# Kernel tuning notes

Hardware: AMD Instinct MI355X
Metric: run time of the kernel (lower is better)

Reference implementation:

```python
import jax, jax.numpy as jnp
import numpy as np

N_NODES = 50000
N_EDGES = 800000
D_IN = 64
D_OUT = 64


def setup_inputs() -> dict:
    key = jax.random.key(0)
    k1, k2, k3, k4, k5 = jax.random.split(key, 5)
    x = jax.random.normal(k1, (N_NODES, D_IN), dtype=jnp.float32)
    senders = jax.random.randint(k2, (N_EDGES,), 0, N_NODES, dtype=jnp.int32)
    receivers = jax.random.randint(k3, (N_EDGES,), 0, N_NODES, dtype=jnp.int32)
    # eqx.nn.Linear params: weight [out, in], bias [out]
    weight = jax.random.normal(k4, (D_OUT, D_IN), dtype=jnp.float32) / np.sqrt(D_IN)
    bias = jax.random.normal(k5, (D_OUT,), dtype=jnp.float32) * 0.01
    return {"x": x, "senders": senders, "receivers": receivers, "weight": weight, "bias": bias}


def reference(x, senders, receivers, weight, bias):
    n = x.shape[0]
    # jraph.GraphConvolution applies update_node_fn (the Linear) FIRST
    h = x @ weight.T + bias  # [N, D_OUT]
    # add self edges
    self_idx = jnp.arange(n, dtype=senders.dtype)
    cs = jnp.concatenate([senders, self_idx])
    cr = jnp.concatenate([receivers, self_idx])
    ones = jnp.ones(cs.shape, dtype=h.dtype)
    sender_deg = jax.ops.segment_sum(ones, cs, num_segments=n)
    receiver_deg = jax.ops.segment_sum(ones, cr, num_segments=n)
    # symmetric normalization: D^{-1/2} A D^{-1/2}
    h = h * jax.lax.rsqrt(jnp.maximum(sender_deg, 1.0))[:, None]
    h = jax.ops.segment_sum(h[cs], cr, num_segments=n)  # gather -> scatter-add
    h = h * jax.lax.rsqrt(jnp.maximum(receiver_deg, 1.0))[:, None]
    return jax.nn.leaky_relu(h)  # default negative_slope=0.01
```

## Files before the change

### kernel.cpp

```cpp
#include <hip/hip_runtime.h>

#define N_NODES 50000
#define N_EDGES 800000
#define D 64
#define NB 196
#define BSZ 256
#define NSLICE 256
#define SLICE_I4 784
#define E4 (N_EDGES / 4)
#define CAP 52

__device__ __forceinline__ ushort f2bf(float f) {
    unsigned u = __float_as_uint(f);
    unsigned r = u + 0x7fffu + ((u >> 16) & 1u);
    return (ushort)(r >> 16);
}
__device__ __forceinline__ void acc8(const uint4 a, float* acc) {
    acc[0] += __uint_as_float(a.x << 16);
    acc[1] += __uint_as_float(a.x & 0xffff0000u);
    acc[2] += __uint_as_float(a.y << 16);
    acc[3] += __uint_as_float(a.y & 0xffff0000u);
    acc[4] += __uint_as_float(a.z << 16);
    acc[5] += __uint_as_float(a.z & 0xffff0000u);
    acc[6] += __uint_as_float(a.w << 16);
    acc[7] += __uint_as_float(a.w & 0xffff0000u);
}

__global__ __launch_bounds__(1024) void part1_kernel(
        const int* __restrict__ s, const int* __restrict__ r,
        unsigned* __restrict__ prc, unsigned char* __restrict__ psc,
        int* __restrict__ rcnt, int* __restrict__ scnt) {
    __shared__ int rcur[NB], scur[NB];
    const int tid = threadIdx.x, sl = blockIdx.x;
    for (int i = tid; i < NB; i += 1024) { rcur[i] = 0; scur[i] = 0; }
    __syncthreads();

    const size_t cellbase = (size_t)sl * NB * CAP;
    int e4 = sl * SLICE_I4 + tid;
    if (tid < SLICE_I4 && e4 < E4) {
        int4 rv = ((const int4*)r)[e4];
        int4 sv = ((const int4*)s)[e4];
        int ri[4] = {rv.x, rv.y, rv.z, rv.w};
        int si[4] = {sv.x, sv.y, sv.z, sv.w};
        #pragma unroll
        for (int k = 0; k < 4; ++k) {
            int b = ri[k] >> 8;
            int pos = atomicAdd(&rcur[b], 1);
            if (pos < CAP)
                prc[cellbase + (size_t)b * CAP + pos] =
                    ((unsigned)(ri[k] & 255) << 16) | (unsigned)si[k];
            int bs = si[k] >> 8;
            int pos2 = atomicAdd(&scur[bs], 1);
            if (pos2 < CAP)
                psc[cellbase + (size_t)bs * CAP + pos2] = (unsigned char)(si[k] & 255);
        }
    }
    __syncthreads();
    for (int i = tid; i < NB; i += 1024) {
        rcnt[sl * NB + i] = rcur[i];
        scnt[sl * NB + i] = scur[i];
    }
}

__global__ __launch_bounds__(256, 4) void post_kernel(
        const unsigned* __restrict__ prc, const unsigned char* __restrict__ psc,
        const int* __restrict__ rcnt, const int* __restrict__ scnt,
        int* __restrict__ rowoff, ushort* __restrict__ csr16,
        const float* __restrict__ x, const float* __restrict__ w,
        const float* __restrict__ bias, ushort* __restrict__ h16) {
    __shared__ int sc[256];
    __shared__ int h4[BSZ];
    __shared__ float wlds[64 * 68];
    __shared__ float xlds[64 * 68];
    __shared__ float slds[BSZ];
    __shared__ float blds[64];
    const int tid = threadIdx.x;

    if (blockIdx.x >= NB) {
        const int b = blockIdx.x - NB;
        h4[tid] = 0;
        if (tid < 64) blds[tid] = bias[tid];
        __syncthreads();
        {
            int sl = tid;
            int c = scnt[sl * NB + b];
            const unsigned char* cell = psc + (size_t)sl * NB * CAP + (size_t)b * CAP;
            for (int i = 0; i < c; ++i) atomicAdd(&h4[cell[i]], 1);
        }
        __syncthreads();
        slds[tid] = rsqrtf((float)(h4[tid] + 1));
        #pragma unroll
        for (int q = 0; q < 4; ++q) {
            int idx = q * 256 + tid;
            int o = idx >> 4, k4 = idx & 15;
            float4 wv = ((const float4*)w)[idx];
            *(float4*)&wlds[o * 68 + k4 * 4] = wv;
        }
        __syncthreads();

        const int t15 = tid & 15;
        const int g = tid >> 4;
        for (int tile = 0; tile < 4; ++tile) {
            const int nb = b * BSZ + tile * 64;
            #pragma unroll
            for (int q = 0; q < 4; ++q) {
                int idx = q * 256 + tid;
                int nl = idx >> 4, k4 = idx & 15;
                int n = nb + nl;
                float4 xv = (n < N_NODES) ? ((const float4*)x)[n * 16 + k4]
                                          : make_float4(0.f, 0.f, 0.f, 0.f);
                *(float4*)&xlds[nl * 68 + k4 * 4] = xv;
            }
            __syncthreads();

            float acc[4][4];
            #pragma unroll
            for (int i = 0; i < 4; ++i)
                #pragma unroll
                for (int j = 0; j < 4; ++j) acc[i][j] = 0.f;

            #pragma unroll 2
            for (int k4 = 0; k4 < 16; ++k4) {
                float4 wv0 = *(const float4*)&wlds[(t15     ) * 68 + k4 * 4];
                float4 wv1 = *(const float4*)&wlds[(t15 + 16) * 68 + k4 * 4];
                float4 wv2 = *(const float4*)&wlds[(t15 + 32) * 68 + k4 * 4];
                float4 wv3 = *(const float4*)&wlds[(t15 + 48) * 68 + k4 * 4];
                #pragma unroll
                for (int i = 0; i < 4; ++i) {
                    float4 xv = *(const float4*)&xlds[(g * 4 + i) * 68 + k4 * 4];
                    acc[i][0] += xv.x * wv0.x + xv.y * wv0.y + xv.z * wv0.z + xv.w * wv0.w;
                    acc[i][1] += xv.x * wv1.x + xv.y * wv1.y + xv.z * wv1.z + xv.w * wv1.w;
                    acc[i][2] += xv.x * wv2.x + xv.y * wv2.y + xv.z * wv2.z + xv.w * wv2.w;
                    acc[i][3] += xv.x * wv3.x + xv.y * wv3.y + xv.z * wv3.z + xv.w * wv3.w;
                }
            }

            #pragma unroll
            for (int i = 0; i < 4; ++i) {
                int nl = g * 4 + i;
                int n = nb + nl;
                if (n < N_NODES) {
                    float scl = slds[tile * 64 + nl];
                    h16[n * D + t15     ] = f2bf((acc[i][0] + blds[t15     ]) * scl);
                    h16[n * D + t15 + 16] = f2bf((acc[i][1] + blds[t15 + 16]) * scl);
                    h16[n * D + t15 + 32] = f2bf((acc[i][2] + blds[t15 + 32]) * scl);
                    h16[n * D + t15 + 48] = f2bf((acc[i][3] + blds[t15 + 48]) * scl);
                }
            }
            __syncthreads();
        }
        return;
    }

    const int b = blockIdx.x;
    int tot = 0;
    if (tid < NB) {
        for (int sl = 0; sl < NSLICE; ++sl) tot += rcnt[sl * NB + tid];
    }
    sc[tid] = tot;
    __syncthreads();
    for (int o = 1; o < 256; o <<= 1) {
        int u = (tid >= o) ? sc[tid - o] : 0;
        __syncthreads();
        sc[tid] += u;
        __syncthreads();
    }
    const int rb = (b == 0) ? 0 : sc[b - 1];
    __syncthreads();

    h4[tid] = 0;
    __syncthreads();
    {
        int sl = tid;
        int c = rcnt[sl * NB + b];
        const unsigned* cell = prc + (size_t)sl * NB * CAP + (size_t)b * CAP;
        for (int i = 0; i < c; ++i) atomicAdd(&h4[cell[i] >> 16], 1);
    }
    __syncthreads();

    int v = h4[tid];
    sc[tid] = v;
    __syncthreads();
    for (int o = 1; o < 256; o <<= 1) {
        int u = (tid >= o) ? sc[tid - o] : 0;
        __syncthreads();
        sc[tid] += u;
        __syncthreads();
    }
    int excl = sc[tid] - v;
    int n = b * BSZ + tid;
    if (n < N_NODES) rowoff[n] = rb + excl;
    h4[tid] = rb + excl;
    if (b == NB - 1 && tid == 0) rowoff[N_NODES] = N_EDGES;
    __syncthreads();

    {
        int sl = tid;
        int c = rcnt[sl * NB + b];
        const unsigned* cell = prc + (size_t)sl * NB * CAP + (size_t)b * CAP;
        for (int i = 0; i < c; ++i) {
            unsigned pw = cell[i];
            int pos = atomicAdd(&h4[pw >> 16], 1);
            csr16[pos] = (ushort)(pw & 0xffffu);
        }
    }
}

__global__ __launch_bounds__(256) void gather_kernel(
        const ushort* __restrict__ h16, const int* __restrict__ rowoff,
        const ushort* __restrict__ csr16, float* __restrict__ out) {
    const int lane = threadIdx.x & 63;
    const int q = lane & 7;
    const int g = lane >> 3;
    const int n = blockIdx.x * 4 + (threadIdx.x >> 6);
    if (n >= N_NODES) return;

    float acc[8];
    #pragma unroll
    for (int k = 0; k < 8; ++k) acc[k] = 0.f;

    const int base = rowoff[n];
    const int cnt = rowoff[n + 1] - base;

    for (int j0 = 0; j0 < cnt; j0 += 64) {
        int m = cnt - j0; if (m > 64) m = 64;
        int my = (lane < m) ? (int)csr16[base + j0 + lane] : 0;
        int t = 0;
        for (; t + 16 <= m; t += 16) {
            int s0 = __shfl(my, t + g);
            int s1 = __shfl(my, t + 8 + g);
            uint4 a = *(const uint4*)&h16[s0 * D + q * 8];
            uint4 b = *(const uint4*)&h16[s1 * D + q * 8];
            acc8(a, acc);
            acc8(b, acc);
        }
        for (; t < m; t += 8) {
            int e = t + g;
            int ee = (e < m) ? e : 0;
            int s0 = __shfl(my, ee);
            if (e < m) {
                uint4 a = *(const uint4*)&h16[s0 * D + q * 8];
                acc8(a, acc);
            }
        }
    }

    #pragma unroll
    for (int k = 0; k < 8; ++k) acc[k] += __shfl_xor(acc[k], 8);
    #pragma unroll
    for (int k = 0; k < 8; ++k) acc[k] += __shfl_xor(acc[k], 16);
    #pragma unroll
    for (int k = 0; k < 8; ++k) acc[k] += __shfl_xor(acc[k], 32);

    uint4 sv = *(const uint4*)&h16[n * D + q * 8];
    acc8(sv, acc);
    float sc = rsqrtf((float)(cnt + 1));
    float o[8];
    #pragma unroll
    for (int k = 0; k < 8; ++k) {
        float vv = acc[k] * sc;
        o[k] = vv > 0.f ? vv : 0.01f * vv;
    }
    if (g == 0) {
        *(float4*)(out + n * D + q * 8)     = make_float4(o[0], o[1], o[2], o[3]);
    } else if (g == 1) {
        *(float4*)(out + n * D + q * 8 + 4) = make_float4(o[4], o[5], o[6], o[7]);
    }
}

extern "C" void kernel_launch(void* const* d_in, const int* in_sizes, int n_in,
                              void* d_out, int out_size, void* d_ws, size_t ws_size,
                              hipStream_t stream) {
    const float* x       = (const float*)d_in[0];
    const int*   senders = (const int*)d_in[1];
    const int*   recvs   = (const int*)d_in[2];
    const float* weight  = (const float*)d_in[3];
    const float* bias    = (const float*)d_in[4];
    float* out = (float*)d_out;

    char* p = (char*)d_ws;
    auto take = [&](size_t bytes) { char* q = p; p += (bytes + 255) & ~(size_t)255; return q; };
    ushort*        h16    = (ushort*)take((size_t)N_NODES * D * 2);
    unsigned*      prc    = (unsigned*)take((size_t)NSLICE * NB * CAP * 4);
    unsigned char* psc    = (unsigned char*)take((size_t)NSLICE * NB * CAP);
    int*           rcnt   = (int*)take((size_t)NSLICE * NB * 4);
    int*           scnt   = (int*)take((size_t)NSLICE * NB * 4);
    int*           rowoff = (int*)take((size_t)(N_NODES + 1) * 4);
    ushort*        csr16  = (ushort*)take((size_t)N_EDGES * 2);

    hipLaunchKernelGGL(part1_kernel, dim3(NSLICE), dim3(1024), 0, stream,
                       senders, recvs, prc, psc, rcnt, scnt);
    hipLaunchKernelGGL(post_kernel, dim3(2 * NB), dim3(BSZ), 0, stream,
                       prc, psc, rcnt, scnt, rowoff, csr16,
                       x, weight, bias, h16);
    hipLaunchKernelGGL(gather_kernel, dim3((N_NODES + 3) / 4), dim3(256), 0, stream,
                       h16, rowoff, csr16, out);
}
```

Measured before the change: 65.67 us.

## Compact per-slice bucket cells via LDS counting sort before writing to global

The first pass now counts per-bucket edges in shared memory, computes exclusive prefix offsets, scatters the packed edge records into LDS in bucket order, and writes each slice out as one contiguous coalesced block. This replaces the fixed-capacity padded cells (CAP per bucket), which caused scattered global stores and left edges beyond the capacity silently dropped. Later kernels read per-slice bucket offsets from new offset arrays. The change adds two block-wide scans and extra barriers to the first kernel, and uses more LDS per 1024-thread block.

After: 64.22 us. 2.2% less time.

```diff
diff --git a/kernel.cpp b/kernel.cpp
--- a/kernel.cpp
+++ b/kernel.cpp
@@ -6,9 +6,9 @@
 #define NB 196
 #define BSZ 256
 #define NSLICE 256
+#define SLICE_E 3136
 #define SLICE_I4 784
 #define E4 (N_EDGES / 4)
-#define CAP 52
 
 __device__ __forceinline__ ushort f2bf(float f) {
     unsigned u = __float_as_uint(f);
@@ -29,42 +29,86 @@
 __global__ __launch_bounds__(1024) void part1_kernel(
         const int* __restrict__ s, const int* __restrict__ r,
         unsigned* __restrict__ prc, unsigned char* __restrict__ psc,
-        int* __restrict__ rcnt, int* __restrict__ scnt) {
+        int* __restrict__ rcnt, int* __restrict__ scnt,
+        int* __restrict__ roffg, int* __restrict__ soffg) {
+    __shared__ unsigned lprc[SLICE_E];
+    __shared__ unsigned char lpsc[SLICE_E];
     __shared__ int rcur[NB], scur[NB];
+    __shared__ int rof[NB], sof[NB];
+    __shared__ int sc[256];
     const int tid = threadIdx.x, sl = blockIdx.x;
     for (int i = tid; i < NB; i += 1024) { rcur[i] = 0; scur[i] = 0; }
     __syncthreads();
 
-    const size_t cellbase = (size_t)sl * NB * CAP;
     int e4 = sl * SLICE_I4 + tid;
-    if (tid < SLICE_I4 && e4 < E4) {
-        int4 rv = ((const int4*)r)[e4];
-        int4 sv = ((const int4*)s)[e4];
+    const bool act = (tid < SLICE_I4) && (e4 < E4);
+    int4 rv, sv;
+    if (act) {
+        rv = ((const int4*)r)[e4];
+        sv = ((const int4*)s)[e4];
+        atomicAdd(&rcur[rv.x >> 8], 1); atomicAdd(&rcur[rv.y >> 8], 1);
+        atomicAdd(&rcur[rv.z >> 8], 1); atomicAdd(&rcur[rv.w >> 8], 1);
+        atomicAdd(&scur[sv.x >> 8], 1); atomicAdd(&scur[sv.y >> 8], 1);
+        atomicAdd(&scur[sv.z >> 8], 1); atomicAdd(&scur[sv.w >> 8], 1);
+    }
+    __syncthreads();
+
+    int v = 0;
+    if (tid < 256) { v = (tid < NB) ? rcur[tid] : 0; sc[tid] = v; }
+    __syncthreads();
+    for (int o = 1; o < 256; o <<= 1) {
+        int u = 0;
+        if (tid < 256 && tid >= o) u = sc[tid - o];
+        __syncthreads();
+        if (tid < 256) sc[tid] += u;
+        __syncthreads();
+    }
+    if (tid < NB) rof[tid] = sc[tid] - v;
+    __syncthreads();
+    int v2 = 0;
+    if (tid < 256) { v2 = (tid < NB) ? scur[tid] : 0; sc[tid] = v2; }
+    __syncthreads();
+    for (int o = 1; o < 256; o <<= 1) {
+        int u = 0;
+        if (tid < 256 && tid >= o) u = sc[tid - o];
+        __syncthreads();
+        if (tid < 256) sc[tid] += u;
+        __syncthreads();
+    }
+    if (tid < NB) sof[tid] = sc[tid] - v2;
+    __syncthreads();
+
+    if (tid < NB) {
+        rcnt[sl * NB + tid] = rcur[tid];
+        scnt[sl * NB + tid] = scur[tid];
+        roffg[sl * NB + tid] = rof[tid];
+        soffg[sl * NB + tid] = sof[tid];
+    }
+    __syncthreads();
+
+    if (act) {
         int ri[4] = {rv.x, rv.y, rv.z, rv.w};
         int si[4] = {sv.x, sv.y, sv.z, sv.w};
         #pragma unroll
         for (int k = 0; k < 4; ++k) {
-            int b = ri[k] >> 8;
-            int pos = atomicAdd(&rcur[b], 1);
-            if (pos < CAP)
-                prc[cellbase + (size_t)b * CAP + pos] =
-                    ((unsigned)(ri[k] & 255) << 16) | (unsigned)si[k];
-            int bs = si[k] >> 8;
-            int pos2 = atomicAdd(&scur[bs], 1);
-            if (pos2 < CAP)
-                psc[cellbase + (size_t)bs * CAP + pos2] = (unsigned char)(si[k] & 255);
-        }
-    }
-    __syncthreads();
-    for (int i = tid; i < NB; i += 1024) {
-        rcnt[sl * NB + i] = rcur[i];
-        scnt[sl * NB + i] = scur[i];
-    }
+            int pos = atomicAdd(&rof[ri[k] >> 8], 1);
+            lprc[pos] = ((unsigned)(ri[k] & 255) << 16) | (unsigned)si[k];
+            int pos2 = atomicAdd(&sof[si[k] >> 8], 1);
+            lpsc[pos2] = (unsigned char)(si[k] & 255);
+        }
+    }
+    __syncthreads();
+
+    if (tid < SLICE_I4)
+        ((uint4*)(prc + (size_t)sl * SLICE_E))[tid] = ((const uint4*)lprc)[tid];
+    if (tid < SLICE_E / 16)
+        ((uint4*)(psc + (size_t)sl * SLICE_E))[tid] = ((const uint4*)lpsc)[tid];
 }
 
 __global__ __launch_bounds__(256, 4) void post_kernel(
         const unsigned* __restrict__ prc, const unsigned char* __restrict__ psc,
         const int* __restrict__ rcnt, const int* __restrict__ scnt,
+        const int* __restrict__ roffg, const int* __restrict__ soffg,
         int* __restrict__ rowoff, ushort* __restrict__ csr16,
         const float* __restrict__ x, const float* __restrict__ w,
         const float* __restrict__ bias, ushort* __restrict__ h16) {
@@ -84,7 +128,7 @@
         {
             int sl = tid;
             int c = scnt[sl * NB + b];
-            const unsigned char* cell = psc + (size_t)sl * NB * CAP + (size_t)b * CAP;
+            const unsigned char* cell = psc + (size_t)sl * SLICE_E + soffg[sl * NB + b];
             for (int i = 0; i < c; ++i) atomicAdd(&h4[cell[i]], 1);
         }
         __syncthreads();
@@ -173,7 +217,7 @@
     {
         int sl = tid;
         int c = rcnt[sl * NB + b];
-        const unsigned* cell = prc + (size_t)sl * NB * CAP + (size_t)b * CAP;
+        const unsigned* cell = prc + (size_t)sl * SLICE_E + roffg[sl * NB + b];
         for (int i = 0; i < c; ++i) atomicAdd(&h4[cell[i] >> 16], 1);
     }
     __syncthreads();
@@ -197,7 +241,7 @@
     {
         int sl = tid;
         int c = rcnt[sl * NB + b];
-        const unsigned* cell = prc + (size_t)sl * NB * CAP + (size_t)b * CAP;
+        const unsigned* cell = prc + (size_t)sl * SLICE_E + roffg[sl * NB + b];
         for (int i = 0; i < c; ++i) {
             unsigned pw = cell[i];
             int pos = atomicAdd(&h4[pw >> 16], 1);
@@ -281,17 +325,19 @@
     char* p = (char*)d_ws;
     auto take = [&](size_t bytes) { char* q = p; p += (bytes + 255) & ~(size_t)255; return q; };
     ushort*        h16    = (ushort*)take((size_t)N_NODES * D * 2);
-    unsigned*      prc    = (unsigned*)take((size_t)NSLICE * NB * CAP * 4);
-    unsigned char* psc    = (unsigned char*)take((size_t)NSLICE * NB * CAP);
+    unsigned*      prc    = (unsigned*)take((size_t)NSLICE * SLICE_E * 4);
+    unsigned char* psc    = (unsigned char*)take((size_t)NSLICE * SLICE_E);
     int*           rcnt   = (int*)take((size_t)NSLICE * NB * 4);
     int*           scnt   = (int*)take((size_t)NSLICE * NB * 4);
+    int*           roffg  = (int*)take((size_t)NSLICE * NB * 4);
+    int*           soffg  = (int*)take((size_t)NSLICE * NB * 4);
     int*           rowoff = (int*)take((size_t)(N_NODES + 1) * 4);
     ushort*        csr16  = (ushort*)take((size_t)N_EDGES * 2);
 
     hipLaunchKernelGGL(part1_kernel, dim3(NSLICE), dim3(1024), 0, stream,
-                       senders, recvs, prc, psc, rcnt, scnt);
+                       senders, recvs, prc, psc, rcnt, scnt, roffg, soffg);
     hipLaunchKernelGGL(post_kernel, dim3(2 * NB), dim3(BSZ), 0, stream,
-                       prc, psc, rcnt, scnt, rowoff, csr16,
+                       prc, psc, rcnt, scnt, roffg, soffg, rowoff, csr16,
                        x, weight, bias, h16);
     hipLaunchKernelGGL(gather_kernel, dim3((N_NODES + 3) / 4), dim3(256), 0, stream,
                        h16, rowoff, csr16, out);
```
